# Performance work log

Measured on AMD Instinct MI355X. Metric: run time of the kernel, lower is better.

The kernel has to match this reference:

```python
import jax, jax.numpy as jnp
import numpy as np

N_FEA, N_CLASS, N_RULE, BATCH, N_ACTIVE = 256, 64, 32, 8192, 16

def setup_inputs() -> dict:
    key = jax.random.key(0)
    ks = jax.random.split(key, 12)
    F, C, R = N_FEA, N_CLASS, N_RULE
    return {
        "x": jax.random.normal(ks[0], (BATCH, F), jnp.float32),
        "proto": jax.random.normal(ks[1], (R, F), jnp.float32),
        "var": jax.random.normal(ks[2], (R, F), jnp.float32),
        "W1": jax.random.normal(ks[3], (2 * F, F), jnp.float32) / np.sqrt(F),
        "b1": jnp.zeros((2 * F,), jnp.float32),
        "W2": jax.random.normal(ks[4], (F, 2 * F), jnp.float32) / np.sqrt(2 * F),
        "b2": jnp.zeros((F,), jnp.float32),
        "W3": jax.random.normal(ks[5], (1, F), jnp.float32) / np.sqrt(F),
        "b3": jnp.zeros((1,), jnp.float32),
        "Wc": jax.random.normal(ks[6], (R, C, F), jnp.float32) / np.sqrt(F),
        "bc": jnp.zeros((R, C), jnp.float32),
        "rules_idx": jnp.arange(N_ACTIVE, dtype=jnp.int32),
    }

def reference(x, proto, var, W1, b1, W2, b2, W3, b3, Wc, bc, rules_idx):
    # Antecedent: Gaussian membership per rule. mv: [R, B, F]
    v = jnp.clip(var, 0.0001, 0.1)  # torch.clamp(self.var, 0.0001, 0.1)
    mv = jnp.exp(-((x[None, :, :] - proto[:, None, :]) ** 2) / (2.0 * v[:, None, :] ** 2))
    # Shared FS MLP applied to each rule's membership: Linear-ELU-Linear-ELU-Linear
    h = jax.nn.elu(jnp.einsum('rbf,gf->rbg', mv, W1) + b1)   # [R, B, 2F]
    h = jax.nn.elu(jnp.einsum('rbg,fg->rbf', h, W2) + b2)    # [R, B, F]
    fsi = (jnp.einsum('rbf,of->rbo', h, W3) + b3)[:, :, 0].T  # [B, R]
    # Indexed softmax over the active rule subset
    fire_strength = jax.nn.softmax(fsi[:, rules_idx], axis=1)  # [B, K]
    # Consequent: per-rule Linear + ReLU. dp: [R, B, C]
    dp = jax.nn.relu(jnp.einsum('bf,rcf->rbc', x, Wc) + bc[:, None, :])
    # Softmax-weighted sum over active rules
    outputs = jnp.einsum('kbc,bk->bc', dp[rules_idx], fire_strength)  # [B, C]
    return (outputs, fire_strength)
```

## Files before the change

### kernel.cpp

```cpp
#include <hip/hip_runtime.h>
#include <hip/hip_bf16.h>
#include <cstdint>
#include <cstddef>

#define NF 256
#define NG 512
#define NC 64
#define NB 8192
#define NK 16
#define BT 64

typedef __attribute__((ext_vector_type(8))) short short8;
typedef __attribute__((ext_vector_type(4))) float floatx4;

__device__ __forceinline__ unsigned short f2bf(float f) {
    union { float f; unsigned int u; } a; a.f = f;
    unsigned int u = a.u;
    u += 0x7fffu + ((u >> 16) & 1u);
    return (unsigned short)(u >> 16);
}
__device__ __forceinline__ float elu1(float z) {
    return z > 0.0f ? z : (__expf(z) - 1.0f);
}
__device__ __forceinline__ unsigned int pk2bf(float a, float b) {
    __hip_bfloat162 h = __float22bfloat162_rn(make_float2(a, b));
    union { __hip_bfloat162 h; unsigned int u; } cv; cv.h = h; return cv.u;
}

__device__ __forceinline__ void bar_lds() {
    __builtin_amdgcn_sched_barrier(0);
    asm volatile("s_waitcnt lgkmcnt(0)" ::: "memory");
    __builtin_amdgcn_s_barrier();
    __builtin_amdgcn_sched_barrier(0);
}

__global__ __launch_bounds__(256) void conv_kernel(
    const float* __restrict__ W1, const float* __restrict__ W2,
    const float* __restrict__ Wc, unsigned short* __restrict__ wb)
{
    int i = blockIdx.x * 256 + threadIdx.x;
    if (i < 131072) {
        int e = i & 7, l = (i >> 3) & 63, K = (i >> 9) & 7, N = i >> 12;
        int src = (N * 16 + (l & 15)) * NF + K * 32 + (l >> 4) * 8 + e;
        wb[i] = f2bf(W1[src]);
    } else if (i < 262144) {
        int o = i - 131072;
        int e = o & 7, l = (o >> 3) & 63, K = (o >> 9) & 15, N = o >> 13;
        int src = (N * 16 + (l & 15)) * NG + K * 32 + (l >> 4) * 8 + e;
        wb[i] = f2bf(W2[src]);
    } else if (i < 786432) {
        int o = i - 262144;
        int e = o & 7, l = (o >> 3) & 63, K = (o >> 9) & 7, N = (o >> 12) & 3, r = o >> 14;
        int src = (r * NC + N * 16 + (l & 15)) * NF + K * 32 + (l >> 4) * 8 + e;
        wb[i] = f2bf(Wc[src]);
    }
}

__global__ __launch_bounds__(256, 2) void fs_kernel(
    const float* __restrict__ x, const float* __restrict__ proto,
    const float* __restrict__ var, const unsigned short* __restrict__ W1b,
    const float* __restrict__ b1, const unsigned short* __restrict__ W2b,
    const float* __restrict__ b2, const float* __restrict__ W3,
    const float* __restrict__ b3, const int* __restrict__ ridx,
    float* __restrict__ fsi)
{
    extern __shared__ unsigned short smem[];
    __shared__ float part[4][64];
    unsigned short* mv   = smem;
    unsigned short* cbuf = smem + 64 * 256;

    const int t   = threadIdx.x;
    const int pid = blockIdx.x;
    const int lg  = (pid & 7) * 256 + (pid >> 3);
    const int kidx = lg & 15;
    const int tile = lg >> 4;
    const int r    = ridx[kidx];
    const int b0   = tile * BT;

    const int wave = t >> 6, lane = t & 63;
    const int ln = lane & 15, lq = lane >> 4;
    const int sxr = (ln & 7) << 4;

    {
        const int col   = (t & 63) * 4;
        const int colb  = (t & 63) * 8;
        const int rbase = t >> 6;
        const float4 p4 = *(const float4*)(proto + (size_t)r * NF + col);
        float4 v4 = *(const float4*)(var + (size_t)r * NF + col);
        float cx = fminf(fmaxf(v4.x, 1e-4f), 0.1f);
        float cy = fminf(fmaxf(v4.y, 1e-4f), 0.1f);
        float cz = fminf(fmaxf(v4.z, 1e-4f), 0.1f);
        float cw = fminf(fmaxf(v4.w, 1e-4f), 0.1f);
        const float L2E = 1.44269504088896340736f;
        float ix = (0.5f * L2E) / (cx * cx);
        float iy = (0.5f * L2E) / (cy * cy);
        float iz = (0.5f * L2E) / (cz * cz);
        float iw = (0.5f * L2E) / (cw * cw);
#pragma unroll 4
        for (int i = 0; i < 16; ++i) {
            int row = i * 4 + rbase;
            const float4 xv = *(const float4*)(x + (size_t)(b0 + row) * NF + col);
            float dx = xv.x - p4.x, dy = xv.y - p4.y, dz = xv.z - p4.z, dw = xv.w - p4.w;
            uint2 pk;
            pk.x = pk2bf(exp2f(-dx * dx * ix), exp2f(-dy * dy * iy));
            pk.y = pk2bf(exp2f(-dz * dz * iz), exp2f(-dw * dw * iw));
            *(uint2*)((char*)mv + row * 512 + (colb ^ ((row & 7) << 4))) = pk;
        }
    }
    bar_lds();

    floatx4 acc2[4][4];
#pragma unroll
    for (int mi = 0; mi < 4; ++mi)
#pragma unroll
        for (int ni = 0; ni < 4; ++ni) {
            floatx4 z = {0.0f, 0.0f, 0.0f, 0.0f};
            acc2[mi][ni] = z;
        }

#pragma unroll 1
    for (int c = 0; c < 2; ++c) {
        floatx4 acc1[4][4];
#pragma unroll
        for (int mi = 0; mi < 4; ++mi)
#pragma unroll
            for (int ni = 0; ni < 4; ++ni) {
                floatx4 z = {0.0f, 0.0f, 0.0f, 0.0f};
                acc1[mi][ni] = z;
            }
        const unsigned short* w1p = W1b + c * 65536 + wave * 16384 + lane * 8;
#pragma unroll 2
        for (int k0i = 0; k0i < 8; ++k0i) {
            short8 a[4], b[4];
#pragma unroll
            for (int mi = 0; mi < 4; ++mi)
                a[mi] = *(const short8*)(w1p + mi * 4096 + k0i * 512);
#pragma unroll
            for (int ni = 0; ni < 4; ++ni)
                b[ni] = *(const short8*)((const char*)mv + (ni * 16 + ln) * 512
                                         + ((k0i * 64 + lq * 16) ^ sxr));
#pragma unroll
            for (int ni = 0; ni < 4; ++ni)
#pragma unroll
                for (int mi = 0; mi < 4; ++mi)
                    acc1[mi][ni] = __builtin_amdgcn_mfma_f32_16x16x32_bf16(
                        a[mi], b[ni], acc1[mi][ni], 0, 0, 0);
        }
        bar_lds();
#pragma unroll
        for (int mi = 0; mi < 4; ++mi) {
            const int nl = wave * 64 + mi * 16 + lq * 4;
            const float4 b4 = *(const float4*)(b1 + c * 256 + nl);
#pragma unroll
            for (int ni = 0; ni < 4; ++ni) {
                uint2 pk;
                pk.x = pk2bf(elu1(acc1[mi][ni][0] + b4.x),
                             elu1(acc1[mi][ni][1] + b4.y));
                pk.y = pk2bf(elu1(acc1[mi][ni][2] + b4.z),
                             elu1(acc1[mi][ni][3] + b4.w));
                *(uint2*)((char*)cbuf + (ni * 16 + ln) * 512 + ((nl * 2) ^ sxr)) = pk;
            }
        }
        bar_lds();
        const unsigned short* w2p = W2b + wave * 32768 + c * 8 * 512 + lane * 8;
#pragma unroll 2
        for (int k0i = 0; k0i < 8; ++k0i) {
            short8 a[4], b[4];
#pragma unroll
            for (int mi = 0; mi < 4; ++mi)
                a[mi] = *(const short8*)(w2p + mi * 8192 + k0i * 512);
#pragma unroll
            for (int ni = 0; ni < 4; ++ni)
                b[ni] = *(const short8*)((const char*)cbuf + (ni * 16 + ln) * 512
                                         + ((k0i * 64 + lq * 16) ^ sxr));
#pragma unroll
            for (int ni = 0; ni < 4; ++ni)
#pragma unroll
                for (int mi = 0; mi < 4; ++mi)
                    acc2[mi][ni] = __builtin_amdgcn_mfma_f32_16x16x32_bf16(
                        a[mi], b[ni], acc2[mi][ni], 0, 0, 0);
        }
    }

    float w3v[4][4], b2v[4][4];
#pragma unroll
    for (int mi = 0; mi < 4; ++mi) {
        const int np = wave * 64 + mi * 16 + lq * 4;
        const float4 wv = *(const float4*)(W3 + np);
        const float4 bv = *(const float4*)(b2 + np);
        w3v[mi][0] = wv.x; w3v[mi][1] = wv.y; w3v[mi][2] = wv.z; w3v[mi][3] = wv.w;
        b2v[mi][0] = bv.x; b2v[mi][1] = bv.y; b2v[mi][2] = bv.z; b2v[mi][3] = bv.w;
    }
#pragma unroll
    for (int ni = 0; ni < 4; ++ni) {
        float s = 0.0f;
#pragma unroll
        for (int mi = 0; mi < 4; ++mi)
#pragma unroll
            for (int rg = 0; rg < 4; ++rg)
                s += elu1(acc2[mi][ni][rg] + b2v[mi][rg]) * w3v[mi][rg];
        s += __shfl_xor(s, 16);
        s += __shfl_xor(s, 32);
        if (lq == 0) part[wave][ni * 16 + ln] = s;
    }
    bar_lds();
    if (t < 64) {
        float s = b3[0];
#pragma unroll
        for (int w = 0; w < 4; ++w) s += part[w][t];
        fsi[(size_t)kidx * NB + b0 + t] = s;
    }
}

__global__ __launch_bounds__(512, 4) void cons_kernel(
    const float* __restrict__ x, const unsigned short* __restrict__ Wcb,
    const float* __restrict__ bc, const float* __restrict__ fsi,
    const int* __restrict__ ridx, float* __restrict__ outp,
    float* __restrict__ fire_out)
{
    __shared__ unsigned short xl[16 * 264];
    __shared__ float fire[16][NK];
    __shared__ float pred[4][16][16];

    const int t  = threadIdx.x;
    const int b0 = blockIdx.x * 16;

    int rr[NK];
#pragma unroll
    for (int k = 0; k < NK; ++k) rr[k] = ridx[k];

    {
        int idx = t;
#pragma unroll
        for (int i = 0; i < 2; ++i, idx += 512) {
            int row = idx >> 6, col = (idx & 63) * 4;
            const float4 xv = *(const float4*)(x + (size_t)(b0 + row) * NF + col);
            uint2 pk;
            pk.x = pk2bf(xv.x, xv.y);
            pk.y = pk2bf(xv.z, xv.w);
            *(uint2*)(xl + row * 264 + col) = pk;
        }
    }
    if (t < 256) {
        const int row = t >> 4, k = t & 15;
        float v = fsi[(size_t)k * NB + b0 + row];
        float mx = v;
        mx = fmaxf(mx, __shfl_xor(mx, 1));
        mx = fmaxf(mx, __shfl_xor(mx, 2));
        mx = fmaxf(mx, __shfl_xor(mx, 4));
        mx = fmaxf(mx, __shfl_xor(mx, 8));
        float e = __expf(v - mx);
        float sum = e;
        sum += __shfl_xor(sum, 1);
        sum += __shfl_xor(sum, 2);
        sum += __shfl_xor(sum, 4);
        sum += __shfl_xor(sum, 8);
        float fv = e / sum;
        fire[row][k] = fv;
        fire_out[(size_t)b0 * NK + t] = fv;
    }
    __syncthreads();

    const int wave = t >> 6, lane = t & 63;
    const int ln = lane & 15, lq = lane >> 4;
    const int cg = wave & 3, half = wave >> 2;
    const int nb = cg * 16;

    short8 afr[8];
#pragma unroll
    for (int k0i = 0; k0i < 8; ++k0i)
        afr[k0i] = *(const short8*)(xl + ln * 264 + k0i * 32 + lq * 8);

    floatx4 oacc = {0.0f, 0.0f, 0.0f, 0.0f};
#pragma unroll
    for (int kp = 0; kp < 4; ++kp) {
        const int k0r = half * 8 + kp * 2;
        const int r0 = rr[k0r], r1 = rr[k0r + 1];
        const unsigned short* Wr0 = Wcb + ((size_t)(r0 * 4 + cg) * 8) * 512 + lane * 8;
        const unsigned short* Wr1 = Wcb + ((size_t)(r1 * 4 + cg) * 8) * 512 + lane * 8;
        floatx4 a0 = {0.0f, 0.0f, 0.0f, 0.0f};
        floatx4 a1 = {0.0f, 0.0f, 0.0f, 0.0f};
#pragma unroll
        for (int k0i = 0; k0i < 8; ++k0i) {
            short8 bb0 = *(const short8*)(Wr0 + k0i * 512);
            short8 bb1 = *(const short8*)(Wr1 + k0i * 512);
            a0 = __builtin_amdgcn_mfma_f32_16x16x32_bf16(afr[k0i], bb0, a0, 0, 0, 0);
            a1 = __builtin_amdgcn_mfma_f32_16x16x32_bf16(afr[k0i], bb1, a1, 0, 0, 0);
        }
        const float bias0 = bc[(size_t)r0 * NC + nb + ln];
        const float bias1 = bc[(size_t)r1 * NC + nb + ln];
#pragma unroll
        for (int rg = 0; rg < 4; ++rg) {
            const int row = lq * 4 + rg;
            oacc[rg] += fmaxf(a0[rg] + bias0, 0.0f) * fire[row][k0r]
                      + fmaxf(a1[rg] + bias1, 0.0f) * fire[row][k0r + 1];
        }
    }
    if (half == 1) {
#pragma unroll
        for (int rg = 0; rg < 4; ++rg)
            pred[cg][lq * 4 + rg][ln] = oacc[rg];
    }
    __syncthreads();
    if (half == 0) {
#pragma unroll
        for (int rg = 0; rg < 4; ++rg)
            outp[(size_t)(b0 + lq * 4 + rg) * NC + nb + ln] =
                oacc[rg] + pred[cg][lq * 4 + rg][ln];
    }
}

extern "C" void kernel_launch(void* const* d_in, const int* in_sizes, int n_in,
                              void* d_out, int out_size, void* d_ws, size_t ws_size,
                              hipStream_t stream)
{
    (void)in_sizes; (void)n_in; (void)out_size;
    if (ws_size < 2097152) return;

    const float* x     = (const float*)d_in[0];
    const float* proto = (const float*)d_in[1];
    const float* var   = (const float*)d_in[2];
    const float* W1    = (const float*)d_in[3];
    const float* b1    = (const float*)d_in[4];
    const float* W2    = (const float*)d_in[5];
    const float* b2    = (const float*)d_in[6];
    const float* W3    = (const float*)d_in[7];
    const float* b3    = (const float*)d_in[8];
    const float* Wc    = (const float*)d_in[9];
    const float* bc    = (const float*)d_in[10];
    const int*   ridx  = (const int*)d_in[11];

    unsigned short* wb  = (unsigned short*)d_ws;
    unsigned short* W1b = wb;
    unsigned short* W2b = wb + 131072;
    unsigned short* Wcb = wb + 262144;
    float* fsi = (float*)((char*)d_ws + (size_t)786432 * 2);

    float* outp     = (float*)d_out;
    float* fire_out = outp + (size_t)NB * NC;

    conv_kernel<<<3072, 256, 0, stream>>>(W1, W2, Wc, wb);

    const int fs_lds = 2 * 64 * 256 * 2;
    hipFuncSetAttribute((const void*)fs_kernel,
                        hipFuncAttributeMaxDynamicSharedMemorySize, fs_lds);
    fs_kernel<<<2048, 256, fs_lds, stream>>>(x, proto, var, W1b, b1, W2b, b2,
                                             W3, b3, ridx, fsi);
    cons_kernel<<<512, 512, 0, stream>>>(x, Wcb, bc, fsi, ridx, outp, fire_out);
}
```

Measured before the change: 177.0 us.

## Fuse weight conversion, FS MLP and consequent into one cooperative persistent kernel

Replaces the three separate launches (weight conversion, fire-strength MLP, consequent) with a single cooperative kernel of 512 blocks that uses grid-wide syncs between phases. The FS phase becomes persistent: each block handles one active rule and loops over four 64-row batch tiles, reusing the per-rule proto and variance values it loaded once. The consequent phase runs on 4 waves with no cross-half reduction. The aim is to remove launch gaps and kernel tails, at the cost of grid.sync overhead and fixed occupancy, with the old three-kernel path kept as a fallback if the cooperative launch fails.

```diff
diff --git a/kernel.cpp b/kernel.cpp
--- a/kernel.cpp
+++ b/kernel.cpp
@@ -1,7 +1,10 @@
 #include <hip/hip_runtime.h>
+#include <hip/hip_cooperative_groups.h>
 #include <hip/hip_bf16.h>
 #include <cstdint>
 #include <cstddef>
+
+namespace cg = cooperative_groups;
 
 #define NF 256
 #define NG 512
@@ -34,11 +37,10 @@
     __builtin_amdgcn_sched_barrier(0);
 }
 
-__global__ __launch_bounds__(256) void conv_kernel(
-    const float* __restrict__ W1, const float* __restrict__ W2,
+__device__ __forceinline__ void conv_one(
+    int i, const float* __restrict__ W1, const float* __restrict__ W2,
     const float* __restrict__ Wc, unsigned short* __restrict__ wb)
 {
-    int i = blockIdx.x * 256 + threadIdx.x;
     if (i < 131072) {
         int e = i & 7, l = (i >> 3) & 63, K = (i >> 9) & 7, N = i >> 12;
         int src = (N * 16 + (l & 15)) * NF + K * 32 + (l >> 4) * 8 + e;
@@ -54,6 +56,264 @@
         int src = (r * NC + N * 16 + (l & 15)) * NF + K * 32 + (l >> 4) * 8 + e;
         wb[i] = f2bf(Wc[src]);
     }
+}
+
+__global__ __launch_bounds__(256, 2) void mega_kernel(
+    const float* __restrict__ x, const float* __restrict__ proto,
+    const float* __restrict__ var, const float* __restrict__ W1,
+    const float* __restrict__ b1, const float* __restrict__ W2,
+    const float* __restrict__ b2, const float* __restrict__ W3,
+    const float* __restrict__ b3, const float* __restrict__ Wc,
+    const float* __restrict__ bc, const int* __restrict__ ridx,
+    unsigned short* __restrict__ W1b, unsigned short* __restrict__ W2b,
+    unsigned short* __restrict__ Wcb, float* __restrict__ fsi,
+    float* __restrict__ outp, float* __restrict__ fire_out)
+{
+    extern __shared__ unsigned short smem[];
+    __shared__ float part[4][64];
+    cg::grid_group grid = cg::this_grid();
+
+    const int t   = threadIdx.x;
+    const int pid = blockIdx.x;
+
+#pragma unroll 1
+    for (int i = pid * 256 + t; i < 786432; i += 512 * 256)
+        conv_one(i, W1, W2, Wc, W1b);
+    grid.sync();
+
+    unsigned short* mv   = smem;
+    unsigned short* cbuf = smem + 64 * 256;
+
+    const int lg    = (pid & 7) * 64 + (pid >> 3);
+    const int kidx  = lg & 15;
+    const int stile = lg >> 4;
+    const int r     = ridx[kidx];
+
+    const int wave = t >> 6, lane = t & 63;
+    const int ln = lane & 15, lq = lane >> 4;
+    const int sxr = (ln & 7) << 4;
+
+    const int col   = (t & 63) * 4;
+    const int colb  = (t & 63) * 8;
+    const int rbase = t >> 6;
+    const float4 p4 = *(const float4*)(proto + (size_t)r * NF + col);
+    float ix, iy, iz, iw;
+    {
+        float4 v4 = *(const float4*)(var + (size_t)r * NF + col);
+        float cx = fminf(fmaxf(v4.x, 1e-4f), 0.1f);
+        float cy = fminf(fmaxf(v4.y, 1e-4f), 0.1f);
+        float cz = fminf(fmaxf(v4.z, 1e-4f), 0.1f);
+        float cw = fminf(fmaxf(v4.w, 1e-4f), 0.1f);
+        const float L2E = 1.44269504088896340736f;
+        ix = (0.5f * L2E) / (cx * cx);
+        iy = (0.5f * L2E) / (cy * cy);
+        iz = (0.5f * L2E) / (cz * cz);
+        iw = (0.5f * L2E) / (cw * cw);
+    }
+
+#pragma unroll 1
+    for (int it = 0; it < 4; ++it) {
+        const int b0 = stile * 256 + it * BT;
+
+#pragma unroll 4
+        for (int i = 0; i < 16; ++i) {
+            int row = i * 4 + rbase;
+            const float4 xv = *(const float4*)(x + (size_t)(b0 + row) * NF + col);
+            float dx = xv.x - p4.x, dy = xv.y - p4.y, dz = xv.z - p4.z, dw = xv.w - p4.w;
+            uint2 pk;
+            pk.x = pk2bf(exp2f(-dx * dx * ix), exp2f(-dy * dy * iy));
+            pk.y = pk2bf(exp2f(-dz * dz * iz), exp2f(-dw * dw * iw));
+            *(uint2*)((char*)mv + row * 512 + (colb ^ ((row & 7) << 4))) = pk;
+        }
+        bar_lds();
+
+        floatx4 acc2[4][4];
+#pragma unroll
+        for (int mi = 0; mi < 4; ++mi)
+#pragma unroll
+            for (int ni = 0; ni < 4; ++ni) {
+                floatx4 z = {0.0f, 0.0f, 0.0f, 0.0f};
+                acc2[mi][ni] = z;
+            }
+
+#pragma unroll 1
+        for (int c = 0; c < 2; ++c) {
+            floatx4 acc1[4][4];
+#pragma unroll
+            for (int mi = 0; mi < 4; ++mi)
+#pragma unroll
+                for (int ni = 0; ni < 4; ++ni) {
+                    floatx4 z = {0.0f, 0.0f, 0.0f, 0.0f};
+                    acc1[mi][ni] = z;
+                }
+            const unsigned short* w1p = W1b + c * 65536 + wave * 16384 + lane * 8;
+#pragma unroll 2
+            for (int k0i = 0; k0i < 8; ++k0i) {
+                short8 a[4], b[4];
+#pragma unroll
+                for (int mi = 0; mi < 4; ++mi)
+                    a[mi] = *(const short8*)(w1p + mi * 4096 + k0i * 512);
+#pragma unroll
+                for (int ni = 0; ni < 4; ++ni)
+                    b[ni] = *(const short8*)((const char*)mv + (ni * 16 + ln) * 512
+                                             + ((k0i * 64 + lq * 16) ^ sxr));
+#pragma unroll
+                for (int ni = 0; ni < 4; ++ni)
+#pragma unroll
+                    for (int mi = 0; mi < 4; ++mi)
+                        acc1[mi][ni] = __builtin_amdgcn_mfma_f32_16x16x32_bf16(
+                            a[mi], b[ni], acc1[mi][ni], 0, 0, 0);
+            }
+            bar_lds();
+#pragma unroll
+            for (int mi = 0; mi < 4; ++mi) {
+                const int nl = wave * 64 + mi * 16 + lq * 4;
+                const float4 b4 = *(const float4*)(b1 + c * 256 + nl);
+#pragma unroll
+                for (int ni = 0; ni < 4; ++ni) {
+                    uint2 pk;
+                    pk.x = pk2bf(elu1(acc1[mi][ni][0] + b4.x),
+                                 elu1(acc1[mi][ni][1] + b4.y));
+                    pk.y = pk2bf(elu1(acc1[mi][ni][2] + b4.z),
+                                 elu1(acc1[mi][ni][3] + b4.w));
+                    *(uint2*)((char*)cbuf + (ni * 16 + ln) * 512 + ((nl * 2) ^ sxr)) = pk;
+                }
+            }
+            bar_lds();
+            const unsigned short* w2p = W2b + wave * 32768 + c * 8 * 512 + lane * 8;
+#pragma unroll 2
+            for (int k0i = 0; k0i < 8; ++k0i) {
+                short8 a[4], b[4];
+#pragma unroll
+                for (int mi = 0; mi < 4; ++mi)
+                    a[mi] = *(const short8*)(w2p + mi * 8192 + k0i * 512);
+#pragma unroll
+                for (int ni = 0; ni < 4; ++ni)
+                    b[ni] = *(const short8*)((const char*)cbuf + (ni * 16 + ln) * 512
+                                             + ((k0i * 64 + lq * 16) ^ sxr));
+#pragma unroll
+                for (int ni = 0; ni < 4; ++ni)
+#pragma unroll
+                    for (int mi = 0; mi < 4; ++mi)
+                        acc2[mi][ni] = __builtin_amdgcn_mfma_f32_16x16x32_bf16(
+                            a[mi], b[ni], acc2[mi][ni], 0, 0, 0);
+            }
+        }
+
+        float w3v[4][4], b2v[4][4];
+#pragma unroll
+        for (int mi = 0; mi < 4; ++mi) {
+            const int np = wave * 64 + mi * 16 + lq * 4;
+            const float4 wv = *(const float4*)(W3 + np);
+            const float4 bv = *(const float4*)(b2 + np);
+            w3v[mi][0] = wv.x; w3v[mi][1] = wv.y; w3v[mi][2] = wv.z; w3v[mi][3] = wv.w;
+            b2v[mi][0] = bv.x; b2v[mi][1] = bv.y; b2v[mi][2] = bv.z; b2v[mi][3] = bv.w;
+        }
+#pragma unroll
+        for (int ni = 0; ni < 4; ++ni) {
+            float s = 0.0f;
+#pragma unroll
+            for (int mi = 0; mi < 4; ++mi)
+#pragma unroll
+                for (int rg = 0; rg < 4; ++rg)
+                    s += elu1(acc2[mi][ni][rg] + b2v[mi][rg]) * w3v[mi][rg];
+            s += __shfl_xor(s, 16);
+            s += __shfl_xor(s, 32);
+            if (lq == 0) part[wave][ni * 16 + ln] = s;
+        }
+        bar_lds();
+        if (t < 64) {
+            float s = b3[0];
+#pragma unroll
+            for (int w = 0; w < 4; ++w) s += part[w][t];
+            fsi[(size_t)kidx * NB + b0 + t] = s;
+        }
+    }
+    grid.sync();
+
+    {
+        unsigned short* xl  = smem;
+        float*          fire = (float*)(smem + 16 * 264);
+        const int b0c = pid * 16;
+
+        int rr[NK];
+#pragma unroll
+        for (int k = 0; k < NK; ++k) rr[k] = ridx[k];
+
+#pragma unroll
+        for (int i = 0; i < 4; ++i) {
+            int idx = t + i * 256;
+            int row = idx >> 6, cc = (idx & 63) * 4;
+            const float4 xv = *(const float4*)(x + (size_t)(b0c + row) * NF + cc);
+            uint2 pk;
+            pk.x = pk2bf(xv.x, xv.y);
+            pk.y = pk2bf(xv.z, xv.w);
+            *(uint2*)(xl + row * 264 + cc) = pk;
+        }
+        {
+            const int row = t >> 4, k = t & 15;
+            float v = fsi[(size_t)k * NB + b0c + row];
+            float mx = v;
+            mx = fmaxf(mx, __shfl_xor(mx, 1));
+            mx = fmaxf(mx, __shfl_xor(mx, 2));
+            mx = fmaxf(mx, __shfl_xor(mx, 4));
+            mx = fmaxf(mx, __shfl_xor(mx, 8));
+            float e = __expf(v - mx);
+            float sum = e;
+            sum += __shfl_xor(sum, 1);
+            sum += __shfl_xor(sum, 2);
+            sum += __shfl_xor(sum, 4);
+            sum += __shfl_xor(sum, 8);
+            float fv = e / sum;
+            fire[row * 16 + k] = fv;
+            fire_out[(size_t)b0c * NK + t] = fv;
+        }
+        __syncthreads();
+
+        const int nb = wave * 16;
+
+        short8 afr[8];
+#pragma unroll
+        for (int k0i = 0; k0i < 8; ++k0i)
+            afr[k0i] = *(const short8*)(xl + ln * 264 + k0i * 32 + lq * 8);
+
+        floatx4 oacc = {0.0f, 0.0f, 0.0f, 0.0f};
+#pragma unroll
+        for (int kp = 0; kp < 8; ++kp) {
+            const int k0r = kp * 2;
+            const int r0 = rr[k0r], r1 = rr[k0r + 1];
+            const unsigned short* Wr0 = Wcb + ((size_t)(r0 * 4 + wave) * 8) * 512 + lane * 8;
+            const unsigned short* Wr1 = Wcb + ((size_t)(r1 * 4 + wave) * 8) * 512 + lane * 8;
+            floatx4 a0 = {0.0f, 0.0f, 0.0f, 0.0f};
+            floatx4 a1 = {0.0f, 0.0f, 0.0f, 0.0f};
+#pragma unroll
+            for (int k0i = 0; k0i < 8; ++k0i) {
+                short8 bb0 = *(const short8*)(Wr0 + k0i * 512);
+                short8 bb1 = *(const short8*)(Wr1 + k0i * 512);
+                a0 = __builtin_amdgcn_mfma_f32_16x16x32_bf16(afr[k0i], bb0, a0, 0, 0, 0);
+                a1 = __builtin_amdgcn_mfma_f32_16x16x32_bf16(afr[k0i], bb1, a1, 0, 0, 0);
+            }
+            const float bias0 = bc[(size_t)r0 * NC + nb + ln];
+            const float bias1 = bc[(size_t)r1 * NC + nb + ln];
+#pragma unroll
+            for (int rg = 0; rg < 4; ++rg) {
+                const int row = lq * 4 + rg;
+                oacc[rg] += fmaxf(a0[rg] + bias0, 0.0f) * fire[row * 16 + k0r]
+                          + fmaxf(a1[rg] + bias1, 0.0f) * fire[row * 16 + k0r + 1];
+            }
+        }
+#pragma unroll
+        for (int rg = 0; rg < 4; ++rg)
+            outp[(size_t)(b0c + lq * 4 + rg) * NC + nb + ln] = oacc[rg];
+    }
+}
+
+__global__ __launch_bounds__(256) void conv_kernel(
+    const float* __restrict__ W1, const float* __restrict__ W2,
+    const float* __restrict__ Wc, unsigned short* __restrict__ wb)
+{
+    int i = blockIdx.x * 256 + threadIdx.x;
+    conv_one(i, W1, W2, Wc, wb);
 }
 
 __global__ __launch_bounds__(256, 2) void fs_kernel(
@@ -263,8 +523,8 @@
 
     const int wave = t >> 6, lane = t & 63;
     const int ln = lane & 15, lq = lane >> 4;
-    const int cg = wave & 3, half = wave >> 2;
-    const int nb = cg * 16;
+    const int cg2 = wave & 3, half = wave >> 2;
+    const int nb = cg2 * 16;
 
     short8 afr[8];
 #pragma unroll
@@ -276,8 +536,8 @@
     for (int kp = 0; kp < 4; ++kp) {
         const int k0r = half * 8 + kp * 2;
         const int r0 = rr[k0r], r1 = rr[k0r + 1];
-        const unsigned short* Wr0 = Wcb + ((size_t)(r0 * 4 + cg) * 8) * 512 + lane * 8;
-        const unsigned short* Wr1 = Wcb + ((size_t)(r1 * 4 + cg) * 8) * 512 + lane * 8;
+        const unsigned short* Wr0 = Wcb + ((size_t)(r0 * 4 + cg2) * 8) * 512 + lane * 8;
+        const unsigned short* Wr1 = Wcb + ((size_t)(r1 * 4 + cg2) * 8) * 512 + lane * 8;
         floatx4 a0 = {0.0f, 0.0f, 0.0f, 0.0f};
         floatx4 a1 = {0.0f, 0.0f, 0.0f, 0.0f};
 #pragma unroll
@@ -299,14 +559,14 @@
     if (half == 1) {
 #pragma unroll
         for (int rg = 0; rg < 4; ++rg)
-            pred[cg][lq * 4 + rg][ln] = oacc[rg];
+            pred[cg2][lq * 4 + rg][ln] = oacc[rg];
     }
     __syncthreads();
     if (half == 0) {
 #pragma unroll
         for (int rg = 0; rg < 4; ++rg)
             outp[(size_t)(b0 + lq * 4 + rg) * NC + nb + ln] =
-                oacc[rg] + pred[cg][lq * 4 + rg][ln];
+                oacc[rg] + pred[cg2][lq * 4 + rg][ln];
     }
 }
 
@@ -339,12 +599,24 @@
     float* outp     = (float*)d_out;
     float* fire_out = outp + (size_t)NB * NC;
 
-    conv_kernel<<<3072, 256, 0, stream>>>(W1, W2, Wc, wb);
-
-    const int fs_lds = 2 * 64 * 256 * 2;
+    const int lds = 2 * 64 * 256 * 2;
+    hipFuncSetAttribute((const void*)mega_kernel,
+                        hipFuncAttributeMaxDynamicSharedMemorySize, lds);
     hipFuncSetAttribute((const void*)fs_kernel,
-                        hipFuncAttributeMaxDynamicSharedMemorySize, fs_lds);
-    fs_kernel<<<2048, 256, fs_lds, stream>>>(x, proto, var, W1b, b1, W2b, b2,
-                                             W3, b3, ridx, fsi);
-    cons_kernel<<<512, 512, 0, stream>>>(x, Wcb, bc, fsi, ridx, outp, fire_out);
-}
+                        hipFuncAttributeMaxDynamicSharedMemorySize, lds);
+
+    void* args[] = { (void*)&x, (void*)&proto, (void*)&var, (void*)&W1,
+                     (void*)&b1, (void*)&W2, (void*)&b2, (void*)&W3,
+                     (void*)&b3, (void*)&Wc, (void*)&bc, (void*)&ridx,
+                     (void*)&W1b, (void*)&W2b, (void*)&Wcb, (void*)&fsi,
+                     (void*)&outp, (void*)&fire_out };
+    hipError_t err = hipLaunchCooperativeKernel((const void*)mega_kernel,
+                                                dim3(512), dim3(256),
+                                                args, lds, stream);
+    if (err != hipSuccess) {
+        conv_kernel<<<3072, 256, 0, stream>>>(W1, W2, Wc, wb);
+        fs_kernel<<<2048, 256, lds, stream>>>(x, proto, var, W1b, b1, W2b, b2,
+                                              W3, b3, ridx, fsi);
+        cons_kernel<<<512, 512, 0, stream>>>(x, Wcb, bc, fsi, ridx, outp, fire_out);
+    }
+}
```

Measured after the change: 281.4 us. 1.59x slower.
